# Kernel optimization log

Hardware: AMD Instinct MI355X
Metric: run time of the kernel (lower is better)

## Reference

```python
import jax, jax.numpy as jnp
import numpy as np

BATCH, D_IN, D_OUT = 2048, 1024, 4096


def setup_inputs() -> dict:
    key = jax.random.key(0)
    kx, kw = jax.random.split(key)
    x = jax.random.normal(kx, (BATCH, D_IN), dtype=jnp.float32)
    W = jax.random.normal(kw, (D_IN, D_OUT), dtype=jnp.float32)  # nn.Parameter init: N(0,1)
    return {"x": x, "W": W}


def reference(x, W):
    # out[b,o] = -1/2 * sum_i (x[b,i] - W[i,o])^2
    # instead of materializing the [B, O, I] broadcast tensor.
    x_sq = jnp.sum(x * x, axis=1, keepdims=True)          # [B, 1]
    w_sq = jnp.sum(W * W, axis=0, keepdims=True)          # [1, O]
    xw = jnp.matmul(x, W)                                  # [B, O] GEMM
    return -0.5 * (x_sq - 2.0 * xw + w_sq)
```

## Files before the change

kernel.cpp:

```cpp
#include <hip/hip_runtime.h>
#include <stdint.h>

#define BATCH 2048
#define DIN   1024
#define DOUT  4096


__device__ __forceinline__ ushort f2bf(float f) {
    uint32_t u = __float_as_uint(f);
    u += 0x7fffu + ((u >> 16) & 1u);
    return (ushort)(u >> 16);
}

__device__ __forceinline__ void async_copy16(const void* gsrc, void* ldst) {
    __builtin_amdgcn_global_load_lds(
        reinterpret_cast<uint32_t __attribute__((address_space(1)))*>(
            reinterpret_cast<uintptr_t>(gsrc)),
        reinterpret_cast<uint32_t __attribute__((address_space(3)))*>(
            reinterpret_cast<uintptr_t>(ldst)),
        16, 0, 0);
}

typedef __bf16 bf16x8 __attribute__((ext_vector_type(8)));
typedef float  f32x4  __attribute__((ext_vector_type(4)));


__global__ __launch_bounds__(256) void prep_x(const float* __restrict__ x,
                                              ushort* __restrict__ xb,
                                              float* __restrict__ xsq) {
    const int row = blockIdx.x;
    const int t = threadIdx.x;
    const float4 v = *(const float4*)(x + (size_t)row * DIN + t * 4);
    ushort4 pk;
    pk.x = f2bf(v.x); pk.y = f2bf(v.y); pk.z = f2bf(v.z); pk.w = f2bf(v.w);
    *(ushort4*)(xb + (size_t)row * DIN + t * 4) = pk;

    float s = v.x * v.x + v.y * v.y + v.z * v.z + v.w * v.w;
    #pragma unroll
    for (int off = 32; off > 0; off >>= 1) s += __shfl_down(s, off);
    __shared__ float ws[4];
    if ((t & 63) == 0) ws[t >> 6] = s;
    __syncthreads();
    if (t == 0) xsq[row] = ws[0] + ws[1] + ws[2] + ws[3];
}

__global__ __launch_bounds__(256) void prep_w(const float* __restrict__ W,
                                              ushort* __restrict__ wbt,
                                              float* __restrict__ wsq) {
    __shared__ float tile[64][65];
    const int o0 = blockIdx.x * 64;
    const int i0 = blockIdx.y * 64;
    const int tx = threadIdx.x & 63;
    const int ty = threadIdx.x >> 6;

    float ssq = 0.f;
    #pragma unroll
    for (int r = ty; r < 64; r += 4) {
        const float v = W[(size_t)(i0 + r) * DOUT + o0 + tx];
        tile[r][tx] = v;
        ssq += v * v;
    }
    atomicAdd(&wsq[o0 + tx], ssq);
    __syncthreads();
    #pragma unroll
    for (int r = ty; r < 64; r += 4) {
        const float v = tile[tx][r];
        wbt[(size_t)(o0 + r) * DIN + i0 + tx] = f2bf(v);
    }
}

#define BM 128
#define BN 128
#define BK 32

__global__ __launch_bounds__(256, 2) void gemm_bt_epi(
    const ushort* __restrict__ A,
    const ushort* __restrict__ Bt,
    const float* __restrict__ xsq,
    const float* __restrict__ wsq,
    float* __restrict__ out) {
    __shared__ __align__(16) ushort sA[BM * BK];
    __shared__ __align__(16) ushort sB[BN * BK];

    const int tid  = threadIdx.x;
    const int wv   = tid >> 6;
    const int lane = tid & 63;
    const int wr = wv >> 1, wc = wv & 1;
    const int m0 = blockIdx.y * BM;
    const int n0 = blockIdx.x * BN;

    const int st_row = wv * 32 + (lane >> 2);
    const int st_col = (lane & 3) * 8;

    const ushort* agp0 = A  + (size_t)(m0 + st_row)      * DIN + st_col;
    const ushort* agp1 = A  + (size_t)(m0 + st_row + 16) * DIN + st_col;
    const ushort* bgp0 = Bt + (size_t)(n0 + st_row)      * DIN + st_col;
    const ushort* bgp1 = Bt + (size_t)(n0 + st_row + 16) * DIN + st_col;

    ushort* sA0 = &sA[wv * 1024];
    ushort* sA1 = &sA[wv * 1024 + 512];
    ushort* sB0 = &sB[wv * 1024];
    ushort* sB1 = &sB[wv * 1024 + 512];

    f32x4 acc[4][4] = {};

    const int a_row = wr * 64 + (lane & 15);
    const int b_row = wc * 64 + (lane & 15);
    const int kq    = (lane >> 4) * 8;

    for (int kt = 0; kt < DIN; kt += BK) {
        __syncthreads();
        async_copy16(agp0 + kt, sA0);
        async_copy16(agp1 + kt, sA1);
        async_copy16(bgp0 + kt, sB0);
        async_copy16(bgp1 + kt, sB1);
        __syncthreads();

        bf16x8 fa[4], fb[4];
        #pragma unroll
        for (int i = 0; i < 4; ++i)
            fa[i] = *(const bf16x8*)&sA[(a_row + i * 16) * BK + kq];
        #pragma unroll
        for (int i = 0; i < 4; ++i)
            fb[i] = *(const bf16x8*)&sB[(b_row + i * 16) * BK + kq];

        #pragma unroll
        for (int mi = 0; mi < 4; ++mi)
            #pragma unroll
            for (int ni = 0; ni < 4; ++ni)
                acc[mi][ni] = __builtin_amdgcn_mfma_f32_16x16x32_bf16(
                    fa[mi], fb[ni], acc[mi][ni], 0, 0, 0);
    }

    const int er = (lane >> 4) * 4;
    const int ec = lane & 15;
    #pragma unroll
    for (int mi = 0; mi < 4; ++mi) {
        const int row = m0 + wr * 64 + mi * 16 + er;
        #pragma unroll
        for (int ni = 0; ni < 4; ++ni) {
            const int col = n0 + wc * 64 + ni * 16 + ec;
            const float wterm = wsq[col];
            #pragma unroll
            for (int r = 0; r < 4; ++r) {
                out[(size_t)(row + r) * DOUT + col] =
                    acc[mi][ni][r] - 0.5f * (xsq[row + r] + wterm);
            }
        }
    }
}


extern "C" void kernel_launch(void* const* d_in, const int* in_sizes, int n_in,
                              void* d_out, int out_size, void* d_ws, size_t ws_size,
                              hipStream_t stream) {
    const float* x = (const float*)d_in[0];
    const float* W = (const float*)d_in[1];
    float* out = (float*)d_out;

    char* ws = (char*)d_ws;
    ushort* xb  = (ushort*)ws;
    ushort* wbt = (ushort*)(ws + (4u << 20));
    float*  xsq = (float*)(ws + (12u << 20));
    float*  wsq = (float*)(ws + (12u << 20) + (16u << 10));

    hipMemsetAsync(wsq, 0, DOUT * sizeof(float), stream);
    prep_x<<<BATCH, 256, 0, stream>>>(x, xb, xsq);
    prep_w<<<dim3(DOUT / 64, DIN / 64), 256, 0, stream>>>(W, wbt, wsq);
    gemm_bt_epi<<<dim3(DOUT / BN, BATCH / BM), 256, 0, stream>>>(xb, wbt, xsq, wsq, out);
}
```

Before: 111.9 us.

## Swizzle LDS k-chunks, drop wsq atomics/memset, hoist epilogue norm terms

prep_w now has each block cover 256 input rows and write per-slice partial squared norms into a buffer. The GEMM epilogue sums the four partials, which removes the memset launch and the global atomics. The GEMM permutes the 16-byte k-chunk placement per row in both the async LDS stores and the fragment reads, to reduce LDS bank conflicts. The epilogue hoists the halved w-norm terms and reorders loops so each x-norm load is reused across columns. Bigger prep_w blocks mean fewer blocks and less parallelism in that kernel.

```diff
diff --git a/kernel.cpp b/kernel.cpp
--- a/kernel.cpp
+++ b/kernel.cpp
@@ -46,27 +46,34 @@
 
 __global__ __launch_bounds__(256) void prep_w(const float* __restrict__ W,
                                               ushort* __restrict__ wbt,
-                                              float* __restrict__ wsq) {
+                                              float* __restrict__ wsqp) {
     __shared__ float tile[64][65];
     const int o0 = blockIdx.x * 64;
-    const int i0 = blockIdx.y * 64;
+    const int jb = blockIdx.y;
     const int tx = threadIdx.x & 63;
     const int ty = threadIdx.x >> 6;
 
     float ssq = 0.f;
-    #pragma unroll
-    for (int r = ty; r < 64; r += 4) {
-        const float v = W[(size_t)(i0 + r) * DOUT + o0 + tx];
-        tile[r][tx] = v;
-        ssq += v * v;
+    for (int sub = 0; sub < 4; ++sub) {
+        const int i0 = jb * 256 + sub * 64;
+        if (sub) __syncthreads();
+        #pragma unroll
+        for (int r = ty; r < 64; r += 4) {
+            const float v = W[(size_t)(i0 + r) * DOUT + o0 + tx];
+            tile[r][tx] = v;
+            ssq += v * v;
+        }
+        __syncthreads();
+        #pragma unroll
+        for (int r = ty; r < 64; r += 4)
+            wbt[(size_t)(o0 + r) * DIN + i0 + tx] = f2bf(tile[tx][r]);
     }
-    atomicAdd(&wsq[o0 + tx], ssq);
     __syncthreads();
-    #pragma unroll
-    for (int r = ty; r < 64; r += 4) {
-        const float v = tile[tx][r];
-        wbt[(size_t)(o0 + r) * DIN + i0 + tx] = f2bf(v);
-    }
+    tile[ty][tx] = ssq;
+    __syncthreads();
+    if (ty == 0)
+        wsqp[(size_t)jb * DOUT + o0 + tx] =
+            tile[0][tx] + tile[1][tx] + tile[2][tx] + tile[3][tx];
 }
 
 #define BM 128
@@ -77,7 +84,7 @@
     const ushort* __restrict__ A,
     const ushort* __restrict__ Bt,
     const float* __restrict__ xsq,
-    const float* __restrict__ wsq,
+    const float* __restrict__ wsqp,
     float* __restrict__ out) {
     __shared__ __align__(16) ushort sA[BM * BK];
     __shared__ __align__(16) ushort sB[BN * BK];
@@ -90,7 +97,7 @@
     const int n0 = blockIdx.x * BN;
 
     const int st_row = wv * 32 + (lane >> 2);
-    const int st_col = (lane & 3) * 8;
+    const int st_col = (((lane & 3) - (lane >> 3)) & 3) * 8;
 
     const ushort* agp0 = A  + (size_t)(m0 + st_row)      * DIN + st_col;
     const ushort* agp1 = A  + (size_t)(m0 + st_row + 16) * DIN + st_col;
@@ -106,7 +113,7 @@
 
     const int a_row = wr * 64 + (lane & 15);
     const int b_row = wc * 64 + (lane & 15);
-    const int kq    = (lane >> 4) * 8;
+    const int kp    = ((((lane >> 4) + ((lane & 15) >> 1)) & 3)) * 8;
 
     for (int kt = 0; kt < DIN; kt += BK) {
         __syncthreads();
@@ -119,10 +126,10 @@
         bf16x8 fa[4], fb[4];
         #pragma unroll
         for (int i = 0; i < 4; ++i)
-            fa[i] = *(const bf16x8*)&sA[(a_row + i * 16) * BK + kq];
+            fa[i] = *(const bf16x8*)&sA[(a_row + i * 16) * BK + kp];
         #pragma unroll
         for (int i = 0; i < 4; ++i)
-            fb[i] = *(const bf16x8*)&sB[(b_row + i * 16) * BK + kq];
+            fb[i] = *(const bf16x8*)&sB[(b_row + i * 16) * BK + kp];
 
         #pragma unroll
         for (int mi = 0; mi < 4; ++mi)
@@ -134,17 +141,23 @@
 
     const int er = (lane >> 4) * 4;
     const int ec = lane & 15;
+    float wh[4];
+    #pragma unroll
+    for (int ni = 0; ni < 4; ++ni) {
+        const int col = n0 + wc * 64 + ni * 16 + ec;
+        wh[ni] = 0.5f * (wsqp[col] + wsqp[DOUT + col] +
+                         wsqp[2 * DOUT + col] + wsqp[3 * DOUT + col]);
+    }
     #pragma unroll
     for (int mi = 0; mi < 4; ++mi) {
         const int row = m0 + wr * 64 + mi * 16 + er;
         #pragma unroll
-        for (int ni = 0; ni < 4; ++ni) {
-            const int col = n0 + wc * 64 + ni * 16 + ec;
-            const float wterm = wsq[col];
+        for (int r = 0; r < 4; ++r) {
+            const float xh = 0.5f * xsq[row + r];
             #pragma unroll
-            for (int r = 0; r < 4; ++r) {
-                out[(size_t)(row + r) * DOUT + col] =
-                    acc[mi][ni][r] - 0.5f * (xsq[row + r] + wterm);
+            for (int ni = 0; ni < 4; ++ni) {
+                const int col = n0 + wc * 64 + ni * 16 + ec;
+                out[(size_t)(row + r) * DOUT + col] = acc[mi][ni][r] - xh - wh[ni];
             }
         }
     }
@@ -159,13 +172,12 @@
     float* out = (float*)d_out;
 
     char* ws = (char*)d_ws;
-    ushort* xb  = (ushort*)ws;
-    ushort* wbt = (ushort*)(ws + (4u << 20));
-    float*  xsq = (float*)(ws + (12u << 20));
-    float*  wsq = (float*)(ws + (12u << 20) + (16u << 10));
+    ushort* xb   = (ushort*)ws;
+    ushort* wbt  = (ushort*)(ws + (4u << 20));
+    float*  xsq  = (float*)(ws + (12u << 20));
+    float*  wsqp = (float*)(ws + (12u << 20) + (32u << 10));
 
-    hipMemsetAsync(wsq, 0, DOUT * sizeof(float), stream);
     prep_x<<<BATCH, 256, 0, stream>>>(x, xb, xsq);
-    prep_w<<<dim3(DOUT / 64, DIN / 64), 256, 0, stream>>>(W, wbt, wsq);
-    gemm_bt_epi<<<dim3(DOUT / BN, BATCH / BM), 256, 0, stream>>>(xb, wbt, xsq, wsq, out);
+    prep_w<<<dim3(DOUT / 64, 4), 256, 0, stream>>>(W, wbt, wsqp);
+    gemm_bt_epi<<<dim3(DOUT / BN, BATCH / BM), 256, 0, stream>>>(xb, wbt, xsq, wsqp, out);
 }
```

Result: slower. 121.8 us (+8.9%).
